# Optimization experiments

Hardware: AMD Instinct MI355X
Metric: run time of the kernel (lower is better)

## Reference

```python
import jax, jax.numpy as jnp
import numpy as np

B = 2_097_152
IN_DIM = 16
OUT_DIM = 32
N_GROUPS = 4
GROUP = 4


def round_ste(x):
    # torch Round custom Function: round in fwd, identity grad in bwd
    return x + jax.lax.stop_gradient(jnp.round(x) - x)


def sign_ste(x):
    # torch Sign custom Function: sign in fwd, identity grad in bwd
    return x + jax.lax.stop_gradient(jnp.sign(x) - x)


def setup_inputs() -> dict:
    key = jax.random.key(0)
    kx, kw = jax.random.split(key)
    return {
        "x": jax.random.normal(kx, (B, IN_DIM), dtype=jnp.float32),
        "weight": jax.random.normal(kw, (OUT_DIM, IN_DIM), dtype=jnp.float32),
        "scale": jnp.float32(15.0),   # unused in forward (kept for faithfulness)
        "in_max": jnp.float32(0.0),
        "in_min": jnp.float32(10.0),
    }


def reference(x, weight, scale, in_max, in_min):
    w = sign_ste(weight)                      # (O, I) in {-1,0,1}
    w_plus = jax.nn.relu(w)
    w_minus = jax.nn.relu(-w)
    rng = in_max - in_min
    # quantize input to 4-bit levels [0, 15]
    xq = jnp.clip(round_ste((x - in_min) / rng * 15.0), 0.0, 15.0)  # (B, I)
    # bias correction term: (ones * InMin) @ w^T
    bias = (jnp.ones_like(x) * in_min) @ w.T  # (B, O)
    # bit-sliced group GEMMs: 4 groups of K=4, plus/minus weight planes
    xg = xq.reshape(-1, N_GROUPS, GROUP)          # (B, G, K)
    wpg = w_plus.reshape(OUT_DIM, N_GROUPS, GROUP)   # (O, G, K)
    wmg = w_minus.reshape(OUT_DIM, N_GROUPS, GROUP)  # (O, G, K)
    yp = jnp.einsum('bgk,ogk->bgo', xg, wpg)      # (B, G, O)
    ym = jnp.einsum('bgk,ogk->bgo', xg, wmg)      # (B, G, O)
    # per-slice requantization: clip(round(y/15), -4, 4), summed over groups
    terms = (jnp.clip(round_ste(yp / 15.0), -4.0, 4.0)
             + jnp.clip(round_ste(-ym / 15.0), -4.0, 4.0))  # (B, G, O)
    out = terms.sum(axis=1) * rng + bias          # (B, O)
    return out
```

## Files before the change

### kernel.cpp

```cpp
#include <hip/hip_runtime.h>
#include <stdint.h>

#define THREADS 256
#define ROWS_PER_BLOCK 256

typedef float nfloat4 __attribute__((ext_vector_type(4)));

#if __has_builtin(__builtin_amdgcn_udot4)
__device__ __forceinline__ uint32_t dot4acc(uint32_t a, uint32_t m, uint32_t c) {
  return __builtin_amdgcn_udot4(a, m, c, false);
}
#else
__device__ __forceinline__ uint32_t dot4acc(uint32_t a, uint32_t m, uint32_t c) {
  uint32_t mf = m;
  mf |= mf << 1;
  mf |= mf << 2;
  mf |= mf << 4;
  uint32_t t = a & mf;
  uint32_t u = (t & 0xFFFFu) + (t >> 16);
  return (u & 0xFFu) + ((u >> 8) & 0xFFu) + c;
}
#endif

__device__ __forceinline__ float quant1(float v, float in_min, float rng) {
  float t = (v - in_min) / rng * 15.0f;
  t = rintf(t);
  t = fmaxf(t, 0.0f);
  t = fminf(t, 15.0f);
  return t;
}

__device__ __forceinline__ uint32_t quant4(float4 v, float in_min, float rng) {
  uint32_t a = (uint32_t)quant1(v.x, in_min, rng);
  uint32_t b = (uint32_t)quant1(v.y, in_min, rng);
  uint32_t c = (uint32_t)quant1(v.z, in_min, rng);
  uint32_t d = (uint32_t)quant1(v.w, in_min, rng);
  return a | (b << 8) | (c << 16) | (d << 24);
}

__global__ __launch_bounds__(THREADS, 6) void quantlinear_kernel(
    const float* __restrict__ x, const float* __restrict__ weight,
    const float* __restrict__ p_in_max, const float* __restrict__ p_in_min,
    float* __restrict__ out, int rows) {
  __shared__ __align__(16) uint4 sh_mp[32];
  __shared__ __align__(16) uint4 sh_mm[32];
  __shared__ __align__(16) float sh_bias[32];
  __shared__ __align__(16) uint32_t sh_xq[ROWS_PER_BLOCK * 4];

  const float in_max = p_in_max[0];
  const float in_min = p_in_min[0];
  const float rng = in_max - in_min;

  const int t = threadIdx.x;

  if (t < 128) {
    const int o = t >> 2, g = t & 3;
    float4 w4 = ((const float4*)weight)[o * 4 + g];
    uint32_t mp = (w4.x > 0.f ? 1u : 0u) | ((w4.y > 0.f ? 1u : 0u) << 8) |
                  ((w4.z > 0.f ? 1u : 0u) << 16) | ((w4.w > 0.f ? 1u : 0u) << 24);
    uint32_t mm = (w4.x < 0.f ? 1u : 0u) | ((w4.y < 0.f ? 1u : 0u) << 8) |
                  ((w4.z < 0.f ? 1u : 0u) << 16) | ((w4.w < 0.f ? 1u : 0u) << 24);
    ((uint32_t*)&sh_mp[o])[g] = mp;
    ((uint32_t*)&sh_mm[o])[g] = mm;
  } else if (t < 160) {
    const int o = t - 128;
    int s = 0;
    for (int i = 0; i < 16; ++i) {
      float w = weight[o * 16 + i];
      s += (w > 0.f) ? 1 : ((w < 0.f) ? -1 : 0);
    }
    sh_bias[o] = in_min * (float)s;
  }

  const float4* __restrict__ xv = (const float4*)x;
  const size_t in_base = (size_t)blockIdx.x * (ROWS_PER_BLOCK * 4);
  const size_t in_lim = (size_t)rows * 4;
#pragma unroll
  for (int s = 0; s < 4; ++s) {
    const int i = s * THREADS + t;
    const size_t gi = in_base + (size_t)i;
    if (gi < in_lim) {
      float4 v = xv[gi];
      sh_xq[i] = quant4(v, in_min, rng);
    }
  }
  __syncthreads();

  const int c = t & 7;

  uint4 mp0 = sh_mp[4 * c + 0], mm0 = sh_mm[4 * c + 0];
  uint4 mp1 = sh_mp[4 * c + 1], mm1 = sh_mm[4 * c + 1];
  uint4 mp2 = sh_mp[4 * c + 2], mm2 = sh_mm[4 * c + 2];
  uint4 mp3 = sh_mp[4 * c + 3], mm3 = sh_mm[4 * c + 3];
  float4 bias4 = ((const float4*)sh_bias)[c];

  nfloat4* __restrict__ outv = (nfloat4*)out;
  const size_t out_base = (size_t)blockIdx.x * (ROWS_PER_BLOCK * 8);
  const size_t out_lim = (size_t)rows * 8;
  const uint4* sh_xq_v = (const uint4*)sh_xq;

#pragma unroll
  for (int s = 0; s < 8; ++s) {
    const int r = (t >> 3) + 32 * s;
    uint4 Xq = sh_xq_v[r];

    float res[4];
#pragma unroll
    for (int j = 0; j < 4; ++j) {
      const uint4 mp = (j == 0) ? mp0 : (j == 1) ? mp1 : (j == 2) ? mp2 : mp3;
      const uint4 mm = (j == 0) ? mm0 : (j == 1) ? mm1 : (j == 2) ? mm2 : mm3;
      int acc = 0;
      {
        uint32_t yp7, ym7;
        yp7 = dot4acc(Xq.x, mp.x, 7u); ym7 = dot4acc(Xq.x, mm.x, 7u);
        acc += (int)((yp7 * 1093u) >> 14) - (int)((ym7 * 1093u) >> 14);
        yp7 = dot4acc(Xq.y, mp.y, 7u); ym7 = dot4acc(Xq.y, mm.y, 7u);
        acc += (int)((yp7 * 1093u) >> 14) - (int)((ym7 * 1093u) >> 14);
        yp7 = dot4acc(Xq.z, mp.z, 7u); ym7 = dot4acc(Xq.z, mm.z, 7u);
        acc += (int)((yp7 * 1093u) >> 14) - (int)((ym7 * 1093u) >> 14);
        yp7 = dot4acc(Xq.w, mp.w, 7u); ym7 = dot4acc(Xq.w, mm.w, 7u);
        acc += (int)((yp7 * 1093u) >> 14) - (int)((ym7 * 1093u) >> 14);
      }
      const float b = (j == 0) ? bias4.x : (j == 1) ? bias4.y
                     : (j == 2) ? bias4.z : bias4.w;
      res[j] = fmaf((float)acc, rng, b);
    }

    const size_t gi = out_base + (size_t)(s * THREADS + t);
    if (gi < out_lim) {
      nfloat4 v = {res[0], res[1], res[2], res[3]};
      __builtin_nontemporal_store(v, &outv[gi]);
    }
  }
}

extern "C" void kernel_launch(void* const* d_in, const int* in_sizes, int n_in,
                              void* d_out, int out_size, void* d_ws, size_t ws_size,
                              hipStream_t stream) {
  const float* x = (const float*)d_in[0];
  const float* w = (const float*)d_in[1];
  const float* in_max = (const float*)d_in[3];
  const float* in_min = (const float*)d_in[4];
  float* out = (float*)d_out;

  const int rows = in_sizes[0] / 16;
  const int blocks = (rows + ROWS_PER_BLOCK - 1) / ROWS_PER_BLOCK;
  quantlinear_kernel<<<blocks, THREADS, 0, stream>>>(x, w, in_max, in_min, out,
                                                     rows);
}
```

Measured before the change: 371.1 us.

## Process four row tiles per block with double-buffered register prefetch

Each block now handles four 256-row tiles instead of one. While it computes and stores the current tile, it prefetches the next tile's input into registers and then quantizes it into a second shared-memory buffer. This spreads the weight-mask and bias setup over more rows and overlaps global loads with compute. In exchange there are four times fewer blocks, more registers per thread and a barrier per tile, which may reduce latency hiding in this memory-bound kernel.

```diff
diff --git a/kernel.cpp b/kernel.cpp
--- a/kernel.cpp
+++ b/kernel.cpp
@@ -2,7 +2,8 @@
 #include <stdint.h>
 
 #define THREADS 256
-#define ROWS_PER_BLOCK 256
+#define TILE_ROWS 256
+#define TILES_PER_BLOCK 4
 
 typedef float nfloat4 __attribute__((ext_vector_type(4)));
 
@@ -45,12 +46,17 @@
   __shared__ __align__(16) uint4 sh_mp[32];
   __shared__ __align__(16) uint4 sh_mm[32];
   __shared__ __align__(16) float sh_bias[32];
-  __shared__ __align__(16) uint32_t sh_xq[ROWS_PER_BLOCK * 4];
+  __shared__ __align__(16) uint32_t sh_xq[2][TILE_ROWS * 4];
+
+  const int nTiles = (rows + TILE_ROWS - 1) / TILE_ROWS;
+  const int tile0 = blockIdx.x * TILES_PER_BLOCK;
+  int myTiles = nTiles - tile0;
+  if (myTiles <= 0) return;
+  if (myTiles > TILES_PER_BLOCK) myTiles = TILES_PER_BLOCK;
 
   const float in_max = p_in_max[0];
   const float in_min = p_in_min[0];
   const float rng = in_max - in_min;
-
   const int t = threadIdx.x;
 
   if (t < 128) {
@@ -73,44 +79,56 @@
   }
 
   const float4* __restrict__ xv = (const float4*)x;
-  const size_t in_base = (size_t)blockIdx.x * (ROWS_PER_BLOCK * 4);
+  nfloat4* __restrict__ outv = (nfloat4*)out;
   const size_t in_lim = (size_t)rows * 4;
+  const size_t out_lim = (size_t)rows * 8;
+
+  float4 pf[4];
 #pragma unroll
   for (int s = 0; s < 4; ++s) {
-    const int i = s * THREADS + t;
-    const size_t gi = in_base + (size_t)i;
-    if (gi < in_lim) {
-      float4 v = xv[gi];
-      sh_xq[i] = quant4(v, in_min, rng);
-    }
+    const size_t gi = (size_t)tile0 * (TILE_ROWS * 4) + s * THREADS + t;
+    pf[s] = (gi < in_lim) ? xv[gi]
+                          : make_float4(in_min, in_min, in_min, in_min);
   }
+#pragma unroll
+  for (int s = 0; s < 4; ++s)
+    sh_xq[0][s * THREADS + t] = quant4(pf[s], in_min, rng);
   __syncthreads();
 
   const int c = t & 7;
-
   uint4 mp0 = sh_mp[4 * c + 0], mm0 = sh_mm[4 * c + 0];
   uint4 mp1 = sh_mp[4 * c + 1], mm1 = sh_mm[4 * c + 1];
   uint4 mp2 = sh_mp[4 * c + 2], mm2 = sh_mm[4 * c + 2];
   uint4 mp3 = sh_mp[4 * c + 3], mm3 = sh_mm[4 * c + 3];
-  float4 bias4 = ((const float4*)sh_bias)[c];
+  const float4 bias4 = ((const float4*)sh_bias)[c];
 
-  nfloat4* __restrict__ outv = (nfloat4*)out;
-  const size_t out_base = (size_t)blockIdx.x * (ROWS_PER_BLOCK * 8);
-  const size_t out_lim = (size_t)rows * 8;
-  const uint4* sh_xq_v = (const uint4*)sh_xq;
+  for (int k = 0; k < myTiles; ++k) {
+    const int tile = tile0 + k;
+    const bool more = (k + 1 < myTiles);
 
+    if (more) {
 #pragma unroll
-  for (int s = 0; s < 8; ++s) {
-    const int r = (t >> 3) + 32 * s;
-    uint4 Xq = sh_xq_v[r];
+      for (int s = 0; s < 4; ++s) {
+        const size_t gi =
+            (size_t)(tile + 1) * (TILE_ROWS * 4) + s * THREADS + t;
+        pf[s] = (gi < in_lim) ? xv[gi]
+                              : make_float4(in_min, in_min, in_min, in_min);
+      }
+    }
 
-    float res[4];
+    const uint4* xqv = (const uint4*)sh_xq[k & 1];
+    const size_t out_base = (size_t)tile * (TILE_ROWS * 8);
 #pragma unroll
-    for (int j = 0; j < 4; ++j) {
-      const uint4 mp = (j == 0) ? mp0 : (j == 1) ? mp1 : (j == 2) ? mp2 : mp3;
-      const uint4 mm = (j == 0) ? mm0 : (j == 1) ? mm1 : (j == 2) ? mm2 : mm3;
-      int acc = 0;
-      {
+    for (int s = 0; s < 8; ++s) {
+      const int r = (t >> 3) + 32 * s;
+      uint4 Xq = xqv[r];
+
+      float res[4];
+#pragma unroll
+      for (int j = 0; j < 4; ++j) {
+        const uint4 mp = (j == 0) ? mp0 : (j == 1) ? mp1 : (j == 2) ? mp2 : mp3;
+        const uint4 mm = (j == 0) ? mm0 : (j == 1) ? mm1 : (j == 2) ? mm2 : mm3;
+        int acc = 0;
         uint32_t yp7, ym7;
         yp7 = dot4acc(Xq.x, mp.x, 7u); ym7 = dot4acc(Xq.x, mm.x, 7u);
         acc += (int)((yp7 * 1093u) >> 14) - (int)((ym7 * 1093u) >> 14);
@@ -120,16 +138,23 @@
         acc += (int)((yp7 * 1093u) >> 14) - (int)((ym7 * 1093u) >> 14);
         yp7 = dot4acc(Xq.w, mp.w, 7u); ym7 = dot4acc(Xq.w, mm.w, 7u);
         acc += (int)((yp7 * 1093u) >> 14) - (int)((ym7 * 1093u) >> 14);
+        const float b = (j == 0) ? bias4.x : (j == 1) ? bias4.y
+                       : (j == 2) ? bias4.z : bias4.w;
+        res[j] = fmaf((float)acc, rng, b);
       }
-      const float b = (j == 0) ? bias4.x : (j == 1) ? bias4.y
-                     : (j == 2) ? bias4.z : bias4.w;
-      res[j] = fmaf((float)acc, rng, b);
+
+      const size_t gi = out_base + (size_t)(s * THREADS + t);
+      if (gi < out_lim) {
+        nfloat4 v = {res[0], res[1], res[2], res[3]};
+        __builtin_nontemporal_store(v, &outv[gi]);
+      }
     }
 
-    const size_t gi = out_base + (size_t)(s * THREADS + t);
-    if (gi < out_lim) {
-      nfloat4 v = {res[0], res[1], res[2], res[3]};
-      __builtin_nontemporal_store(v, &outv[gi]);
+    if (more) {
+#pragma unroll
+      for (int s = 0; s < 4; ++s)
+        sh_xq[(k + 1) & 1][s * THREADS + t] = quant4(pf[s], in_min, rng);
+      __syncthreads();
     }
   }
 }
@@ -144,7 +169,8 @@
   float* out = (float*)d_out;
 
   const int rows = in_sizes[0] / 16;
-  const int blocks = (rows + ROWS_PER_BLOCK - 1) / ROWS_PER_BLOCK;
+  const int tiles = (rows + TILE_ROWS - 1) / TILE_ROWS;
+  const int blocks = (tiles + TILES_PER_BLOCK - 1) / TILES_PER_BLOCK;
   quantlinear_kernel<<<blocks, THREADS, 0, stream>>>(x, w, in_max, in_min, out,
                                                      rows);
 }
```

Measured after the change: 386.7 us. 4.2% more time.
